# Optimization experiments

Measured on AMD Instinct MI355X. Metric: run time of the kernel, lower is better.

Reference implementation:

```python
import jax, jax.numpy as jnp
import numpy as np

N = 100000
E = 3200000
DI = 256
DO = 256
BN_EPS = 1e-5


def _bn_relu(h, gamma, beta):
    # BatchNorm1d in training mode: biased batch stats over the node axis.
    mean = jnp.mean(h, axis=0)
    var = jnp.var(h, axis=0)  # biased, as torch uses for normalization
    hn = (h - mean) * jax.lax.rsqrt(var + BN_EPS)
    return jax.nn.relu(hn * gamma + beta)


def setup_inputs() -> dict:
    key = jax.random.key(0)
    ks = jax.random.split(key, 6)
    x = jax.random.normal(ks[0], (N, DI), dtype=jnp.float32)
    edge_row = jax.random.randint(ks[1], (E,), 0, N, dtype=jnp.int32)
    edge_col = jax.random.randint(ks[2], (E,), 0, N, dtype=jnp.int32)
    edge_vals = jnp.ones((E,), dtype=jnp.float32)
    eps = jnp.zeros((1,), dtype=jnp.float32)
    W1 = jax.random.normal(ks[3], (DI, DO), dtype=jnp.float32) * 0.05
    b1 = jnp.zeros((DO,), dtype=jnp.float32)
    g1 = jnp.ones((DO,), dtype=jnp.float32)
    be1 = jnp.zeros((DO,), dtype=jnp.float32)
    W2 = jax.random.normal(ks[4], (DO, DO), dtype=jnp.float32) * 0.05
    b2 = jnp.zeros((DO,), dtype=jnp.float32)
    g2 = jnp.ones((DO,), dtype=jnp.float32)
    be2 = jnp.zeros((DO,), dtype=jnp.float32)
    return {"x": x, "edge_row": edge_row, "edge_col": edge_col, "edge_vals": edge_vals,
            "eps": eps, "W1": W1, "b1": b1, "g1": g1, "be1": be1,
            "W2": W2, "b2": b2, "g2": g2, "be2": be2}


def reference(x, edge_row, edge_col, edge_vals, eps, W1, b1, g1, be1, W2, b2, g2, be2):
    n = x.shape[0]
    # SpMM: agg[i] = sum_{e: row[e]==i} vals[e] * x[col[e]]
    msgs = edge_vals[:, None] * x[edge_col]          # [E, di]
    agg = jax.ops.segment_sum(msgs, edge_row, num_segments=n)  # [N, di]
    h = (1.0 + eps[0]) * x + agg                      # self-loop combine
    h = _bn_relu(h @ W1 + b1, g1, be1)
    h = _bn_relu(h @ W2 + b2, g2, be2)
    return h
```

## Files before the change

kernel.cpp:

```cpp
#include <hip/hip_runtime.h>

typedef float f32x4 __attribute__((ext_vector_type(4)));
typedef __bf16 bf16x8 __attribute__((ext_vector_type(8)));

#define NBIN_MAX 512
#define CH 6144

__device__ __forceinline__ unsigned short f2b(float f) {
    unsigned int x = __float_as_uint(f);
    unsigned int r = x + 0x7FFFu + ((x >> 16) & 1u);
    return (unsigned short)(r >> 16);
}
__device__ __forceinline__ float blo(unsigned int d) { return __uint_as_float(d << 16); }
__device__ __forceinline__ float bhi(unsigned int d) { return __uint_as_float(d & 0xffff0000u); }

__device__ __forceinline__ void gload_lds16(const void* g, void* l) {
    __builtin_amdgcn_global_load_lds((const __attribute__((address_space(1))) void*)g,
                                     (__attribute__((address_space(3))) void*)l, 16, 0, 0);
}

__global__ __launch_bounds__(256) void prep_kernel(const float* __restrict__ x, unsigned short* __restrict__ xb, int total8,
                                                   const float* __restrict__ W1, const float* __restrict__ W2,
                                                   unsigned short* __restrict__ w1t, unsigned short* __restrict__ w2t,
                                                   const int* __restrict__ er, int* __restrict__ bin_hist, int E,
                                                   int nconv, int nhist, int nbin) {
    __shared__ int lh[NBIN_MAX];
    int b = blockIdx.x, t = threadIdx.x;
    if (b < nconv) {
        int gid = b * 256 + t;
        if (gid >= total8) return;
        size_t idx = (size_t)gid * 8;
        float4 v0 = *(const float4*)(x + idx);
        float4 v1 = *(const float4*)(x + idx + 4);
        ushort4 o0, o1;
        o0.x = f2b(v0.x); o0.y = f2b(v0.y); o0.z = f2b(v0.z); o0.w = f2b(v0.w);
        o1.x = f2b(v1.x); o1.y = f2b(v1.y); o1.z = f2b(v1.z); o1.w = f2b(v1.w);
        *(ushort4*)(xb + idx) = o0;
        *(ushort4*)(xb + idx + 4) = o1;
    } else if (b < nconv + 512) {
        int gid = (b - nconv) * 256 + t;
        int which = gid >> 16;
        int idx = gid & 65535;
        int n = idx >> 8, k = idx & 255;
        const float* W = which ? W2 : W1;
        unsigned short* O = which ? w2t : w1t;
        O[n * 256 + k] = f2b(W[k * 256 + n]);
    } else {
        for (int i = t; i < NBIN_MAX; i += 256) lh[i] = 0;
        __syncthreads();
        int e0 = (b - nconv - 512) * 256 + t;
        int step = nhist * 256;
        for (int e = e0; e < E; e += step)
            atomicAdd(&lh[er[e] >> 8], 1);
        __syncthreads();
        for (int i = t; i < nbin; i += 256) {
            int h = lh[i];
            if (h) atomicAdd(&bin_hist[i], h);
        }
    }
}

__global__ __launch_bounds__(512) void bin_scan_kernel(const int* __restrict__ bin_hist, int* __restrict__ bin_start,
                                                       int* __restrict__ bin_cursor, int* __restrict__ row_start,
                                                       int nbin, int N, int E) {
    __shared__ int wsum[8];
    int t = threadIdx.x, lane = t & 63, w = t >> 6;
    int v = (t < nbin) ? bin_hist[t] : 0;
    int inc = v;
#pragma unroll
    for (int off = 1; off < 64; off <<= 1) {
        int u = __shfl_up(inc, off);
        if (lane >= off) inc += u;
    }
    if (lane == 63) wsum[w] = inc;
    __syncthreads();
    int woff = 0;
    for (int i = 0; i < w; ++i) woff += wsum[i];
    int excl = woff + inc - v;
    if (t < nbin) { bin_start[t] = excl; bin_cursor[t] = excl; }
    if (t == 0) { bin_start[nbin] = E; row_start[N] = E; }
}

__global__ __launch_bounds__(512) void scatter1_kernel(const int* __restrict__ er, const int* __restrict__ ec,
                                                       const float* __restrict__ ev, int* __restrict__ bin_cursor,
                                                       int2* __restrict__ cvt, int E, int nbin) {
    __shared__ int hist[NBIN_MAX];
    __shared__ int lstart[NBIN_MAX];
    __shared__ int gbase[NBIN_MAX];
    __shared__ int lcur[NBIN_MAX];
    __shared__ int2 stage[CH];
    __shared__ unsigned short binof[CH];
    __shared__ int wsum[8];

    const int t = threadIdx.x;
    const int e0 = blockIdx.x * CH;
    const int ecnt = min(CH, E - e0);

    for (int i = t; i < nbin; i += 512) hist[i] = 0;
    __syncthreads();
    for (int i = t; i < ecnt; i += 512)
        atomicAdd(&hist[er[e0 + i] >> 8], 1);
    __syncthreads();
    {
        int lane = t & 63, w = t >> 6;
        int a = (2 * t < nbin) ? hist[2 * t] : 0;
        int b2 = (2 * t + 1 < nbin) ? hist[2 * t + 1] : 0;
        int s = a + b2;
        int inc = s;
#pragma unroll
        for (int off = 1; off < 64; off <<= 1) {
            int u = __shfl_up(inc, off);
            if (lane >= off) inc += u;
        }
        if (lane == 63) wsum[w] = inc;
        __syncthreads();
        int woff = 0;
        for (int i = 0; i < w; ++i) woff += wsum[i];
        int excl = woff + inc - s;
        if (2 * t < nbin) { lstart[2 * t] = excl; lcur[2 * t] = excl; }
        if (2 * t + 1 < nbin) { lstart[2 * t + 1] = excl + a; lcur[2 * t + 1] = excl + a; }
    }
    for (int i = t; i < nbin; i += 512) {
        int h = hist[i];
        gbase[i] = h ? atomicAdd(&bin_cursor[i], h) : 0;
    }
    __syncthreads();
    for (int i = t; i < ecnt; i += 512) {
        int r = er[e0 + i], c = ec[e0 + i];
        float v = ev[e0 + i];
        int bin = r >> 8;
        int q = atomicAdd(&lcur[bin], 1);
        stage[q] = make_int2(c | ((r & 255) << 20), __float_as_int(v));
        binof[q] = (unsigned short)bin;
    }
    __syncthreads();
    for (int q = t; q < ecnt; q += 512) {
        int bin = binof[q];
        int gpos = gbase[bin] + (q - lstart[bin]);
        cvt[gpos] = stage[q];
    }
}

__global__ __launch_bounds__(256) void scatter2_kernel(const int2* __restrict__ cvt, const int* __restrict__ bin_start,
                                                       int* __restrict__ row_start, int2* __restrict__ cv, int N) {
    __shared__ int lhist[256];
    __shared__ int lcur[256];
    __shared__ int wsum[4];
    const int b = blockIdx.x, t = threadIdx.x;
    const int r0 = b * 256;
    const int estart = bin_start[b];
    const int eend = bin_start[b + 1];
    lhist[t] = 0;
    __syncthreads();
    for (int i = estart + t; i < eend; i += 256)
        atomicAdd(&lhist[cvt[i].x >> 20], 1);
    __syncthreads();
    int lane = t & 63, w = t >> 6;
    int v = lhist[t];
    int inc = v;
#pragma unroll
    for (int off = 1; off < 64; off <<= 1) {
        int u = __shfl_up(inc, off);
        if (lane >= off) inc += u;
    }
    if (lane == 63) wsum[w] = inc;
    __syncthreads();
    int woff = 0;
    for (int i = 0; i < w; ++i) woff += wsum[i];
    int excl = estart + woff + inc - v;
    int r = r0 + t;
    if (r < N) row_start[r] = excl;
    lcur[t] = excl;
    __syncthreads();
    for (int i = estart + t; i < eend; i += 256) {
        int2 d = cvt[i];
        int lrow = d.x >> 20;
        int pos = atomicAdd(&lcur[lrow], 1);
        cv[pos] = make_int2(d.x & 0xFFFFF, d.y);
    }
}

template <int HALF>
__global__ __launch_bounds__(256) void spmm_half_kernel(const unsigned short* __restrict__ xb, const int2* __restrict__ cv,
                                                        const int* __restrict__ row_start,
                                                        const float* __restrict__ epsp, unsigned short* __restrict__ h0, int N) {
    int node = blockIdx.x * 4 + (threadIdx.x >> 6);
    int lane = threadIdx.x & 63;
    if (node >= N) return;
    int start = __builtin_amdgcn_readfirstlane(row_start[node]);
    int deg   = __builtin_amdgcn_readfirstlane(row_start[node + 1]) - start;
    const char* xbb = (const char*)xb;
    const int half = lane >> 5;
    const int voff = (lane & 31) * 8 + HALF * 256;
    float a0 = 0.f, a1 = 0.f, a2 = 0.f, a3 = 0.f;

#define PAIR(j0)                                                                 \
    {                                                                            \
        int cA = __builtin_amdgcn_readlane(my.x, (j0));                          \
        int cB = __builtin_amdgcn_readlane(my.x, (j0) + 1);                      \
        float vA = __int_as_float(__builtin_amdgcn_readlane(my.y, (j0)));        \
        float vB = __int_as_float(__builtin_amdgcn_readlane(my.y, (j0) + 1));    \
        int col = half ? cB : cA;                                                \
        float val = half ? vB : vA;                                              \
        uint2 d = *(const uint2*)(xbb + (size_t)col * 512 + voff);               \
        a0 += val * blo(d.x); a1 += val * bhi(d.x);                              \
        a2 += val * blo(d.y); a3 += val * bhi(d.y);                              \
    }

    for (int base = 0; base < deg; base += 64) {
        int rem = deg - base; if (rem > 64) rem = 64;
        long long pk = 0;
        if (lane < rem) pk = __builtin_nontemporal_load((const long long*)(cv + start + base + lane));
        int2 my = make_int2((int)(pk & 0xffffffffLL), (int)(pk >> 32));
        int j = 0;
        for (; j + 8 <= rem; j += 8) { PAIR(j); PAIR(j + 2); PAIR(j + 4); PAIR(j + 6); }
        for (; j < rem; j += 2) PAIR(j);
    }
#undef PAIR

    a0 += __shfl_xor(a0, 32);
    a1 += __shfl_xor(a1, 32);
    a2 += __shfl_xor(a2, 32);
    a3 += __shfl_xor(a3, 32);

    if (lane < 32) {
        float ep = 1.0f + epsp[0];
        uint2 xo = *(const uint2*)(xbb + (size_t)node * 512 + voff);
        unsigned int w0 = ((unsigned int)f2b(ep * blo(xo.x) + a0)) | (((unsigned int)f2b(ep * bhi(xo.x) + a1)) << 16);
        unsigned int w1 = ((unsigned int)f2b(ep * blo(xo.y) + a2)) | (((unsigned int)f2b(ep * bhi(xo.y) + a3)) << 16);
        unsigned long long ov = (unsigned long long)w0 | ((unsigned long long)w1 << 32);
        __builtin_nontemporal_store(ov, (unsigned long long*)((char*)h0 + (size_t)node * 512 + voff));
    }
}

template <int MODE>
__global__ __launch_bounds__(512, 4) void gemm_bn_kernel(const unsigned short* __restrict__ A,
                                                         const unsigned short* __restrict__ Wt,
                                                         const float* __restrict__ bias,
                                                         const float* __restrict__ statsIn,
                                                         const float* __restrict__ gIn,
                                                         const float* __restrict__ beIn,
                                                         float invN,
                                                         unsigned short* __restrict__ Y,
                                                         float* __restrict__ stats, int N) {
    __shared__ unsigned short As[128 * 64];
    __shared__ unsigned short Bs[256 * 64];
    __shared__ float red[8][2][128];
    __shared__ float cf[512];

    const int t = threadIdx.x, lane = t & 63, w = t >> 6;
    const int wm = w >> 1, wn = w & 1;
    const long row0 = (long)blockIdx.x * 128;

    f32x4 acc[2][8];
#pragma unroll
    for (int i = 0; i < 2; ++i)
#pragma unroll
        for (int j = 0; j < 8; ++j) acc[i][j] = (f32x4){0.f, 0.f, 0.f, 0.f};

    const int lr8 = lane >> 3;
    const int sb8 = (lane & 7) << 4;

    uint4 rA[2][2];
    const int slot = t & 7;
    const int rri[2] = { t >> 3, (t + 512) >> 3 };
    if (MODE == 1) {
        if (t < 256) {
            float mean = statsIn[t] * invN;
            float var = statsIn[256 + t] * invN - mean * mean;
            float rs = rsqrtf(var + 1e-5f);
            float a = gIn[t] * rs;
            cf[t] = a;
            cf[256 + t] = beIn[t] - mean * a;
        }
#pragma unroll
        for (int i = 0; i < 2; ++i)
            rA[0][i] = *(const uint4*)(A + (row0 + rri[i]) * 256 + slot * 8);
        __syncthreads();
    }

#pragma unroll
    for (int ks = 0; ks < 4; ++ks) {
        if (ks) __syncthreads();
        if (MODE == 0) {
#pragma unroll
            for (int i = 0; i < 2; ++i) {
                int chunk = w * 2 + i;
                int r = chunk * 8 + lr8;
                int sb = sb8 ^ ((r & 7) << 4);
                gload_lds16(A + (row0 + r) * 256 + ks * 64 + (sb >> 1), (char*)As + chunk * 1024);
            }
        }
#pragma unroll
        for (int i = 0; i < 4; ++i) {
            int chunk = w * 4 + i;
            int n = chunk * 8 + lr8;
            int sb = sb8 ^ ((n & 7) << 4);
            gload_lds16(Wt + n * 256 + ks * 64 + (sb >> 1), (char*)Bs + chunk * 1024);
        }
        if (MODE == 1) {
            int k = ks * 64 + slot * 8;
            float4 a0 = *(const float4*)(cf + k);
            float4 a1 = *(const float4*)(cf + k + 4);
            float4 c0 = *(const float4*)(cf + 256 + k);
            float4 c1 = *(const float4*)(cf + 256 + k + 4);
            float av[8] = {a0.x, a0.y, a0.z, a0.w, a1.x, a1.y, a1.z, a1.w};
            float cvf[8] = {c0.x, c0.y, c0.z, c0.w, c1.x, c1.y, c1.z, c1.w};
#pragma unroll
            for (int i = 0; i < 2; ++i) {
                uint4 v = rA[ks & 1][i];
                unsigned int dw[4] = {v.x, v.y, v.z, v.w};
                unsigned int ov[4];
#pragma unroll
                for (int q = 0; q < 4; ++q) {
                    float o0 = fmaxf(0.f, blo(dw[q]) * av[2 * q] + cvf[2 * q]);
                    float o1 = fmaxf(0.f, bhi(dw[q]) * av[2 * q + 1] + cvf[2 * q + 1]);
                    ov[q] = (unsigned int)f2b(o0) | ((unsigned int)f2b(o1) << 16);
                }
                uint4 ovv = {ov[0], ov[1], ov[2], ov[3]};
                int r = rri[i];
                *(uint4*)((char*)As + r * 128 + ((slot << 4) ^ ((r & 7) << 4))) = ovv;
            }
        }
        __syncthreads();
        if (MODE == 1 && ks < 3) {
#pragma unroll
            for (int i = 0; i < 2; ++i)
                rA[(ks + 1) & 1][i] = *(const uint4*)(A + (row0 + rri[i]) * 256 + (ks + 1) * 64 + slot * 8);
        }
#pragma unroll
        for (int k2 = 0; k2 < 2; ++k2) {
            int cb = k2 * 64 + ((lane >> 4) << 4);
            bf16x8 af[2];
#pragma unroll
            for (int mf = 0; mf < 2; ++mf) {
                int r = wm * 32 + mf * 16 + (lane & 15);
                af[mf] = *(const bf16x8*)((const char*)As + r * 128 + (cb ^ ((r & 7) << 4)));
            }
#pragma unroll
            for (int nf = 0; nf < 8; ++nf) {
                int n = wn * 128 + nf * 16 + (lane & 15);
                bf16x8 bfr = *(const bf16x8*)((const char*)Bs + n * 128 + (cb ^ ((n & 7) << 4)));
                acc[0][nf] = __builtin_amdgcn_mfma_f32_16x16x32_bf16(af[0], bfr, acc[0][nf], 0, 0, 0);
                acc[1][nf] = __builtin_amdgcn_mfma_f32_16x16x32_bf16(af[1], bfr, acc[1][nf], 0, 0, 0);
            }
        }
    }

    float csum[8], csq[8];
#pragma unroll
    for (int nf = 0; nf < 8; ++nf) { csum[nf] = 0.f; csq[nf] = 0.f; }
#pragma unroll
    for (int nf = 0; nf < 8; ++nf) {
        int col = wn * 128 + nf * 16 + (lane & 15);
        float b = bias[col];
#pragma unroll
        for (int mf = 0; mf < 2; ++mf) {
#pragma unroll
            for (int reg = 0; reg < 4; ++reg) {
                long r = row0 + wm * 32 + mf * 16 + ((lane >> 4) << 2) + reg;
                if (r < N) {
                    float y = acc[mf][nf][reg] + b;
                    Y[r * 256 + col] = f2b(y);
                    csum[nf] += y;
                    csq[nf] += y * y;
                }
            }
        }
    }
#pragma unroll
    for (int nf = 0; nf < 8; ++nf) {
        csum[nf] += __shfl_xor(csum[nf], 16);
        csum[nf] += __shfl_xor(csum[nf], 32);
        csq[nf] += __shfl_xor(csq[nf], 16);
        csq[nf] += __shfl_xor(csq[nf], 32);
    }
    if (lane < 16) {
#pragma unroll
        for (int nf = 0; nf < 8; ++nf) {
            red[w][0][nf * 16 + lane] = csum[nf];
            red[w][1][nf * 16 + lane] = csq[nf];
        }
    }
    __syncthreads();
    if (t < 256) {
        int wnc = t >> 7, cc = t & 127;
        float s = 0.f, q = 0.f;
#pragma unroll
        for (int m = 0; m < 4; ++m) {
            s += red[m * 2 + wnc][0][cc];
            q += red[m * 2 + wnc][1][cc];
        }
        atomicAdd(&stats[t], s);
        atomicAdd(&stats[256 + t], q);
    }
}

__global__ __launch_bounds__(256) void bnrelu_out_kernel(const unsigned short* __restrict__ y,
                                                         const float* __restrict__ statsIn,
                                                         const float* __restrict__ gIn,
                                                         const float* __restrict__ beIn,
                                                         float invN,
                                                         float* __restrict__ out, int total) {
    __shared__ float cf[512];
    int t = threadIdx.x;
    {
        float mean = statsIn[t] * invN;
        float var = statsIn[256 + t] * invN - mean * mean;
        float rs = rsqrtf(var + 1e-5f);
        float a = gIn[t] * rs;
        cf[t] = a;
        cf[256 + t] = beIn[t] - mean * a;
    }
    __syncthreads();
    int gid = blockIdx.x * 256 + t;
    if (gid >= total) return;
    int r = gid >> 5, s = gid & 31;
    size_t idx = (size_t)r * 256 + s * 8;
    uint4 v = *(const uint4*)(y + idx);
    float4 a0 = *(const float4*)(cf + s * 8);
    float4 a1 = *(const float4*)(cf + s * 8 + 4);
    float4 c0 = *(const float4*)(cf + 256 + s * 8);
    float4 c1 = *(const float4*)(cf + 256 + s * 8 + 4);
    unsigned int vv[4] = {v.x, v.y, v.z, v.w};
    float av[8] = {a0.x, a0.y, a0.z, a0.w, a1.x, a1.y, a1.z, a1.w};
    float cvf[8] = {c0.x, c0.y, c0.z, c0.w, c1.x, c1.y, c1.z, c1.w};
    float o[8];
#pragma unroll
    for (int j = 0; j < 4; ++j) {
        o[2 * j]     = fmaxf(0.f, blo(vv[j]) * av[2 * j] + cvf[2 * j]);
        o[2 * j + 1] = fmaxf(0.f, bhi(vv[j]) * av[2 * j + 1] + cvf[2 * j + 1]);
    }
    float4 w0 = {o[0], o[1], o[2], o[3]};
    float4 w1 = {o[4], o[5], o[6], o[7]};
    *(float4*)(out + idx) = w0;
    *(float4*)(out + idx + 4) = w1;
}

extern "C" void kernel_launch(void* const* d_in, const int* in_sizes, int n_in,
                              void* d_out, int out_size, void* d_ws, size_t ws_size,
                              hipStream_t stream) {
    const float* x   = (const float*)d_in[0];
    const int*   er  = (const int*)d_in[1];
    const int*   ec  = (const int*)d_in[2];
    const float* ev  = (const float*)d_in[3];
    const float* eps = (const float*)d_in[4];
    const float* W1  = (const float*)d_in[5];
    const float* b1  = (const float*)d_in[6];
    const float* g1  = (const float*)d_in[7];
    const float* be1 = (const float*)d_in[8];
    const float* W2  = (const float*)d_in[9];
    const float* b2  = (const float*)d_in[10];
    const float* g2  = (const float*)d_in[11];
    const float* be2 = (const float*)d_in[12];

    const int N = in_sizes[0] / 256;
    const int E = in_sizes[1];
    const int Npad = ((N + 127) / 128) * 128;
    const int nbin = (N + 255) >> 8;

    char* ws = (char*)d_ws;
    size_t off = 0;
    auto alloc = [&](size_t bytes) { size_t cur = off; off = (off + bytes + 255) & ~(size_t)255; return cur; };
    size_t o_stats  = alloc(4096);
    size_t o_binh   = alloc(NBIN_MAX * 4);
    size_t zbytes   = off;
    size_t o_rowst  = alloc((size_t)(N + 1) * 4);
    size_t o_bins   = alloc((NBIN_MAX + 1) * 4);
    size_t o_binc   = alloc(NBIN_MAX * 4);
    size_t o_cv     = alloc((size_t)E * 8);
    size_t o_xb     = alloc((size_t)N * 256 * 2);
    size_t o_h0     = alloc((size_t)Npad * 256 * 2);
    size_t o_y1     = alloc((size_t)Npad * 256 * 2);
    size_t o_w1t    = alloc(65536 * 2);
    size_t o_w2t    = alloc(65536 * 2);
    (void)ws_size;

    float* stats = (float*)(ws + o_stats);
    int* bin_hist = (int*)(ws + o_binh);
    int* row_start = (int*)(ws + o_rowst);
    int* bin_start = (int*)(ws + o_bins);
    int* bin_cursor = (int*)(ws + o_binc);
    int2* cv = (int2*)(ws + o_cv);
    unsigned short* xb = (unsigned short*)(ws + o_xb);
    unsigned short* h0 = (unsigned short*)(ws + o_h0);
    unsigned short* y1 = (unsigned short*)(ws + o_y1);
    int2* cvt = (int2*)(ws + o_y1);
    unsigned short* w1t = (unsigned short*)(ws + o_w1t);
    unsigned short* w2t = (unsigned short*)(ws + o_w2t);

    hipMemsetAsync(ws, 0, zbytes, stream);

    int total8 = N * 32;
    int nconv = (total8 + 255) / 256;
    int nhist = 256;
    prep_kernel<<<nconv + 512 + nhist, 256, 0, stream>>>(x, xb, total8, W1, W2, w1t, w2t,
                                                         er, bin_hist, E, nconv, nhist, nbin);

    bin_scan_kernel<<<1, 512, 0, stream>>>(bin_hist, bin_start, bin_cursor, row_start, nbin, N, E);

    scatter1_kernel<<<(E + CH - 1) / CH, 512, 0, stream>>>(er, ec, ev, bin_cursor, cvt, E, nbin);
    scatter2_kernel<<<nbin, 256, 0, stream>>>(cvt, bin_start, row_start, cv, N);

    spmm_half_kernel<0><<<(N + 3) / 4, 256, 0, stream>>>(xb, cv, row_start, eps, h0, N);
    spmm_half_kernel<1><<<(N + 3) / 4, 256, 0, stream>>>(xb, cv, row_start, eps, h0, N);

    float invN = 1.0f / (float)N;
    gemm_bn_kernel<0><<<Npad / 128, 512, 0, stream>>>(h0, w1t, b1, nullptr, nullptr, nullptr, 0.f,
                                                      y1, stats, N);
    gemm_bn_kernel<1><<<Npad / 128, 512, 0, stream>>>(y1, w2t, b2, stats, g1, be1, invN,
                                                      h0, stats + 512, N);
    bnrelu_out_kernel<<<(total8 + 255) / 256, 256, 0, stream>>>(h0, stats + 512, g2, be2, invN,
                                                                (float*)d_out, total8);
}
```

Baseline: 483.2 us.

## Merge SpMM halves into one launch, register-stage A in GEMM, nontemporal streaming

Measured after the change: 467.1 us. 1.03x faster.

```diff
diff --git a/kernel.cpp b/kernel.cpp
--- a/kernel.cpp
+++ b/kernel.cpp
@@ -1,6 +1,7 @@
 #include <hip/hip_runtime.h>
 
 typedef float f32x4 __attribute__((ext_vector_type(4)));
+typedef unsigned int uintx4 __attribute__((ext_vector_type(4)));
 typedef __bf16 bf16x8 __attribute__((ext_vector_type(8)));
 
 #define NBIN_MAX 512
@@ -30,13 +31,14 @@
         int gid = b * 256 + t;
         if (gid >= total8) return;
         size_t idx = (size_t)gid * 8;
-        float4 v0 = *(const float4*)(x + idx);
-        float4 v1 = *(const float4*)(x + idx + 4);
-        ushort4 o0, o1;
-        o0.x = f2b(v0.x); o0.y = f2b(v0.y); o0.z = f2b(v0.z); o0.w = f2b(v0.w);
-        o1.x = f2b(v1.x); o1.y = f2b(v1.y); o1.z = f2b(v1.z); o1.w = f2b(v1.w);
-        *(ushort4*)(xb + idx) = o0;
-        *(ushort4*)(xb + idx + 4) = o1;
+        uintx4 u0 = __builtin_nontemporal_load((const uintx4*)(x + idx));
+        uintx4 u1 = __builtin_nontemporal_load((const uintx4*)(x + idx + 4));
+        uintx4 o;
+        o.x = (unsigned int)f2b(__uint_as_float(u0.x)) | ((unsigned int)f2b(__uint_as_float(u0.y)) << 16);
+        o.y = (unsigned int)f2b(__uint_as_float(u0.z)) | ((unsigned int)f2b(__uint_as_float(u0.w)) << 16);
+        o.z = (unsigned int)f2b(__uint_as_float(u1.x)) | ((unsigned int)f2b(__uint_as_float(u1.y)) << 16);
+        o.w = (unsigned int)f2b(__uint_as_float(u1.z)) | ((unsigned int)f2b(__uint_as_float(u1.w)) << 16);
+        __builtin_nontemporal_store(o, (uintx4*)(xb + idx));
     } else if (b < nconv + 512) {
         int gid = (b - nconv) * 256 + t;
         int which = gid >> 16;
@@ -180,18 +182,20 @@
     }
 }
 
-template <int HALF>
-__global__ __launch_bounds__(256) void spmm_half_kernel(const unsigned short* __restrict__ xb, const int2* __restrict__ cv,
-                                                        const int* __restrict__ row_start,
-                                                        const float* __restrict__ epsp, unsigned short* __restrict__ h0, int N) {
-    int node = blockIdx.x * 4 + (threadIdx.x >> 6);
+__global__ __launch_bounds__(256) void spmm_kernel(const unsigned short* __restrict__ xb, const int2* __restrict__ cv,
+                                                   const int* __restrict__ row_start,
+                                                   const float* __restrict__ epsp, unsigned short* __restrict__ h0,
+                                                   int N, int nblk) {
+    int bid = blockIdx.x;
+    int hsel = (bid >= nblk) ? 1 : 0;
+    int node = (bid - hsel * nblk) * 4 + (threadIdx.x >> 6);
     int lane = threadIdx.x & 63;
     if (node >= N) return;
     int start = __builtin_amdgcn_readfirstlane(row_start[node]);
     int deg   = __builtin_amdgcn_readfirstlane(row_start[node + 1]) - start;
     const char* xbb = (const char*)xb;
     const int half = lane >> 5;
-    const int voff = (lane & 31) * 8 + HALF * 256;
+    const int voff = (lane & 31) * 8 + hsel * 256;
     float a0 = 0.f, a1 = 0.f, a2 = 0.f, a3 = 0.f;
 
 #define PAIR(j0)                                                                 \
@@ -264,33 +268,23 @@
     uint4 rA[2][2];
     const int slot = t & 7;
     const int rri[2] = { t >> 3, (t + 512) >> 3 };
-    if (MODE == 1) {
-        if (t < 256) {
-            float mean = statsIn[t] * invN;
-            float var = statsIn[256 + t] * invN - mean * mean;
-            float rs = rsqrtf(var + 1e-5f);
-            float a = gIn[t] * rs;
-            cf[t] = a;
-            cf[256 + t] = beIn[t] - mean * a;
-        }
-#pragma unroll
-        for (int i = 0; i < 2; ++i)
-            rA[0][i] = *(const uint4*)(A + (row0 + rri[i]) * 256 + slot * 8);
-        __syncthreads();
-    }
+    if (MODE == 1 && t < 256) {
+        float mean = statsIn[t] * invN;
+        float var = statsIn[256 + t] * invN - mean * mean;
+        float rs = rsqrtf(var + 1e-5f);
+        float a = gIn[t] * rs;
+        cf[t] = a;
+        cf[256 + t] = beIn[t] - mean * a;
+    }
+#pragma unroll
+    for (int i = 0; i < 2; ++i)
+        rA[0][i] = *(const uint4*)(A + (row0 + rri[i]) * 256 + slot * 8);
+    if (MODE == 1) __syncthreads();
 
 #pragma unroll
     for (int ks = 0; ks < 4; ++ks) {
+        const int p = ks & 1;
         if (ks) __syncthreads();
-        if (MODE == 0) {
-#pragma unroll
-            for (int i = 0; i < 2; ++i) {
-                int chunk = w * 2 + i;
-                int r = chunk * 8 + lr8;
-                int sb = sb8 ^ ((r & 7) << 4);
-                gload_lds16(A + (row0 + r) * 256 + ks * 64 + (sb >> 1), (char*)As + chunk * 1024);
-            }
-        }
 #pragma unroll
         for (int i = 0; i < 4; ++i) {
             int chunk = w * 4 + i;
@@ -298,35 +292,38 @@
             int sb = sb8 ^ ((n & 7) << 4);
             gload_lds16(Wt + n * 256 + ks * 64 + (sb >> 1), (char*)Bs + chunk * 1024);
         }
-        if (MODE == 1) {
-            int k = ks * 64 + slot * 8;
-            float4 a0 = *(const float4*)(cf + k);
-            float4 a1 = *(const float4*)(cf + k + 4);
-            float4 c0 = *(const float4*)(cf + 256 + k);
-            float4 c1 = *(const float4*)(cf + 256 + k + 4);
-            float av[8] = {a0.x, a0.y, a0.z, a0.w, a1.x, a1.y, a1.z, a1.w};
-            float cvf[8] = {c0.x, c0.y, c0.z, c0.w, c1.x, c1.y, c1.z, c1.w};
-#pragma unroll
-            for (int i = 0; i < 2; ++i) {
-                uint4 v = rA[ks & 1][i];
-                unsigned int dw[4] = {v.x, v.y, v.z, v.w};
-                unsigned int ov[4];
+#pragma unroll
+        for (int i = 0; i < 2; ++i) {
+            uint4 v = rA[p][i];
+            unsigned int dw[4] = {v.x, v.y, v.z, v.w};
+            unsigned int ov[4];
+            if (MODE == 1) {
+                int k = ks * 64 + slot * 8;
+                float4 a0 = *(const float4*)(cf + k);
+                float4 a1 = *(const float4*)(cf + k + 4);
+                float4 c0 = *(const float4*)(cf + 256 + k);
+                float4 c1 = *(const float4*)(cf + 256 + k + 4);
+                float av[8] = {a0.x, a0.y, a0.z, a0.w, a1.x, a1.y, a1.z, a1.w};
+                float cvf[8] = {c0.x, c0.y, c0.z, c0.w, c1.x, c1.y, c1.z, c1.w};
 #pragma unroll
                 for (int q = 0; q < 4; ++q) {
                     float o0 = fmaxf(0.f, blo(dw[q]) * av[2 * q] + cvf[2 * q]);
                     float o1 = fmaxf(0.f, bhi(dw[q]) * av[2 * q + 1] + cvf[2 * q + 1]);
                     ov[q] = (unsigned int)f2b(o0) | ((unsigned int)f2b(o1) << 16);
                 }
-                uint4 ovv = {ov[0], ov[1], ov[2], ov[3]};
-                int r = rri[i];
-                *(uint4*)((char*)As + r * 128 + ((slot << 4) ^ ((r & 7) << 4))) = ovv;
+            } else {
+#pragma unroll
+                for (int q = 0; q < 4; ++q) ov[q] = dw[q];
             }
+            uint4 ovv = {ov[0], ov[1], ov[2], ov[3]};
+            int r = rri[i];
+            *(uint4*)((char*)As + r * 128 + ((slot << 4) ^ ((r & 7) << 4))) = ovv;
         }
         __syncthreads();
-        if (MODE == 1 && ks < 3) {
+        if (ks < 3) {
 #pragma unroll
             for (int i = 0; i < 2; ++i)
-                rA[(ks + 1) & 1][i] = *(const uint4*)(A + (row0 + rri[i]) * 256 + (ks + 1) * 64 + slot * 8);
+                rA[p ^ 1][i] = *(const uint4*)(A + (row0 + rri[i]) * 256 + (ks + 1) * 64 + slot * 8);
         }
 #pragma unroll
         for (int k2 = 0; k2 < 2; ++k2) {
@@ -417,7 +414,7 @@
     if (gid >= total) return;
     int r = gid >> 5, s = gid & 31;
     size_t idx = (size_t)r * 256 + s * 8;
-    uint4 v = *(const uint4*)(y + idx);
+    uintx4 v = __builtin_nontemporal_load((const uintx4*)(y + idx));
     float4 a0 = *(const float4*)(cf + s * 8);
     float4 a1 = *(const float4*)(cf + s * 8 + 4);
     float4 c0 = *(const float4*)(cf + 256 + s * 8);
@@ -431,10 +428,10 @@
         o[2 * j]     = fmaxf(0.f, blo(vv[j]) * av[2 * j] + cvf[2 * j]);
         o[2 * j + 1] = fmaxf(0.f, bhi(vv[j]) * av[2 * j + 1] + cvf[2 * j + 1]);
     }
-    float4 w0 = {o[0], o[1], o[2], o[3]};
-    float4 w1 = {o[4], o[5], o[6], o[7]};
-    *(float4*)(out + idx) = w0;
-    *(float4*)(out + idx + 4) = w1;
+    f32x4 w0 = {o[0], o[1], o[2], o[3]};
+    f32x4 w1 = {o[4], o[5], o[6], o[7]};
+    __builtin_nontemporal_store(w0, (f32x4*)(out + idx));
+    __builtin_nontemporal_store(w1, (f32x4*)(out + idx + 4));
 }
 
 extern "C" void kernel_launch(void* const* d_in, const int* in_sizes, int n_in,
@@ -502,8 +499,8 @@
     scatter1_kernel<<<(E + CH - 1) / CH, 512, 0, stream>>>(er, ec, ev, bin_cursor, cvt, E, nbin);
     scatter2_kernel<<<nbin, 256, 0, stream>>>(cvt, bin_start, row_start, cv, N);
 
-    spmm_half_kernel<0><<<(N + 3) / 4, 256, 0, stream>>>(xb, cv, row_start, eps, h0, N);
-    spmm_half_kernel<1><<<(N + 3) / 4, 256, 0, stream>>>(xb, cv, row_start, eps, h0, N);
+    int nblk = (N + 3) / 4;
+    spmm_kernel<<<2 * nblk, 256, 0, stream>>>(xb, cv, row_start, eps, h0, N, nblk);
 
     float invN = 1.0f / (float)N;
     gemm_bn_kernel<0><<<Npad / 128, 512, 0, stream>>>(h0, w1t, b1, nullptr, nullptr, nullptr, 0.f,
```
